# Kernel tuning notes

Hardware: AMD Instinct MI355X
Metric: run time of the kernel (lower is better)

## Reference

```python
import jax, jax.numpy as jnp
import numpy as np

# Mesh/packing dims: deltaV_packed.view(B, M, V, ndims) requires N = B*M*V
B, M, V = 2, 4, 40000
N = B * M * V            # 320_000 packed vertices
E = 960000               # ~3 edges per vertex (triangle mesh)
F_IN = 128               # n_input_features
LAT = 128                # latent_channels
NDIMS = 3
N_HIDDEN = 2             # n_f2f_hidden_layer


def graph_conv(x, edges, W0, b0, W1, b1):
    """pytorch3d-style GraphConv: w0(x) + sum_{j in N(i)} w1(x_j), undirected edges."""
    h0 = x @ W0 + b0                     # self term  [N, out]
    h1 = x @ W1 + b1                     # neighbor messages [N, out]
    src, dst = edges[:, 0], edges[:, 1]
    agg = jnp.zeros_like(h0).at[src].add(h1[dst]).at[dst].add(h1[src])
    return h0 + agg


def setup_inputs() -> dict:
    key = jax.random.key(0)
    ks = jax.random.split(key, 20)
    inp = {
        "features": jax.random.normal(ks[0], (N, F_IN), jnp.float32),
        "edges": jax.random.randint(ks[1], (E, 2), 0, N, dtype=jnp.int32),
    }
    # Layer dims: f2f first (F_IN->LAT), 2 hidden (LAT->LAT), f2v (LAT->NDIMS).
    dims = [(F_IN, LAT), (LAT, LAT), (LAT, LAT), (LAT, NDIMS)]
    for i, (din, dout) in enumerate(dims):
        kk = jax.random.split(ks[2 + i], 4)
        s = 1.0 / np.sqrt(din)
        inp[f"W0_{i}"] = jax.random.normal(kk[0], (din, dout), jnp.float32) * s
        inp[f"b0_{i}"] = jnp.zeros((dout,), jnp.float32)
        inp[f"W1_{i}"] = jax.random.normal(kk[1], (din, dout), jnp.float32) * s
        inp[f"b1_{i}"] = jnp.zeros((dout,), jnp.float32)
    return inp


def reference(features, edges,
              W0_0, b0_0, W1_0, b1_0,
              W0_1, b0_1, W1_1, b1_1,
              W0_2, b0_2, W1_2, b1_2,
              W0_3, b0_3, W1_3, b1_3):
    # Features2FeaturesResidual: first GC + 2 hidden GCs (ReLU each, norm='none'),
    # residual skip (identity since F_IN == LAT).
    h = jax.nn.relu(graph_conv(features, edges, W0_0, b0_0, W1_0, b1_0))
    h = jax.nn.relu(graph_conv(h, edges, W0_1, b0_1, W1_1, b1_1))
    h = jax.nn.relu(graph_conv(h, edges, W0_2, b0_2, W1_2, b1_2))
    h = h + features
    # f2v: GC(latent -> ndims), no activation
    deltaV = graph_conv(h, edges, W0_3, b0_3, W1_3, b1_3)
    return deltaV.reshape(B, M, V, NDIMS)
```

## Files before the change

kernel.cpp:

```cpp
#include <hip/hip_runtime.h>
#include <hip/hip_bf16.h>

#define NNODES 320000
#define NEDGES 960000

typedef __attribute__((ext_vector_type(8))) short short8;
typedef __attribute__((ext_vector_type(4))) float f32x4;

__device__ __forceinline__ float b2f(unsigned short u) {
    return __uint_as_float(((unsigned)u) << 16);
}
__device__ __forceinline__ unsigned short f2b(float f) {
    __hip_bfloat16 h = __float2bfloat16(f);
    union { __hip_bfloat16 h; unsigned short u; } cv;
    cv.h = h;
    return cv.u;
}


__global__ void k_zero(int* p, int n) {
    int i = blockIdx.x * blockDim.x + threadIdx.x;
    int s = gridDim.x * blockDim.x;
    for (; i < n; i += s) p[i] = 0;
}

__global__ void k_count(const int* __restrict__ edges, int* __restrict__ deg) {
    int i = blockIdx.x * blockDim.x + threadIdx.x;
    int s = gridDim.x * blockDim.x;
    for (; i < NEDGES; i += s) {
        int a = edges[2 * i], b = edges[2 * i + 1];
        atomicAdd(&deg[a], 1);
        atomicAdd(&deg[b], 1);
    }
}

#define SCAN_BLOCK 256
#define SCAN_ITEMS 8
#define SCAN_CHUNK 2048
#define SCAN_NB 157

__global__ void k_scan1(const int* __restrict__ deg, int* __restrict__ bsum) {
    __shared__ int sd[SCAN_BLOCK];
    int b = blockIdx.x, t = threadIdx.x;
    int base = b * SCAN_CHUNK + t * SCAN_ITEMS;
    int s = 0;
    for (int i = 0; i < SCAN_ITEMS; i++) {
        int g = base + i;
        if (g < NNODES) s += deg[g];
    }
    sd[t] = s;
    __syncthreads();
    for (int off = 128; off > 0; off >>= 1) {
        if (t < off) sd[t] += sd[t + off];
        __syncthreads();
    }
    if (t == 0) bsum[b] = sd[0];
}

__global__ void k_scan2(int* bsum, int* rowptr) {
    if (blockIdx.x == 0 && threadIdx.x == 0) {
        int run = 0;
        for (int b = 0; b < SCAN_NB; b++) {
            int v = bsum[b];
            bsum[b] = run;
            run += v;
        }
        rowptr[NNODES] = run;
    }
}

__global__ void k_scan3(int* __restrict__ deg_cursor, int* __restrict__ rowptr,
                        const int* __restrict__ bsum, float* __restrict__ degf) {
    __shared__ int sd[SCAN_BLOCK];
    int b = blockIdx.x, t = threadIdx.x;
    int base = b * SCAN_CHUNK + t * SCAN_ITEMS;
    int v[SCAN_ITEMS];
    int s = 0;
    for (int i = 0; i < SCAN_ITEMS; i++) {
        int g = base + i;
        v[i] = (g < NNODES) ? deg_cursor[g] : 0;
        s += v[i];
    }
    sd[t] = s;
    __syncthreads();
    for (int off = 1; off < SCAN_BLOCK; off <<= 1) {
        int x = (t >= off) ? sd[t - off] : 0;
        __syncthreads();
        sd[t] += x;
        __syncthreads();
    }
    int prefix = bsum[b] + (sd[t] - s);
    for (int i = 0; i < SCAN_ITEMS; i++) {
        int g = base + i;
        if (g < NNODES) {
            rowptr[g] = prefix;
            deg_cursor[g] = prefix;
            degf[g] = (float)v[i];
            prefix += v[i];
        }
    }
}

__global__ void k_fill(const int* __restrict__ edges, int* __restrict__ cursor,
                       int* __restrict__ adj) {
    int i = blockIdx.x * blockDim.x + threadIdx.x;
    int s = gridDim.x * blockDim.x;
    for (; i < NEDGES; i += s) {
        int a = edges[2 * i], b = edges[2 * i + 1];
        adj[atomicAdd(&cursor[a], 1)] = b;
        adj[atomicAdd(&cursor[b], 1)] = a;
    }
}


__global__ void k_cvt(const float* __restrict__ f, unsigned short* __restrict__ o,
                      long n4) {
    long i = (long)blockIdx.x * blockDim.x + threadIdx.x;
    long s = (long)gridDim.x * blockDim.x;
    for (; i < n4; i += s) {
        float4 v = *(const float4*)&f[i * 4];
        uint2 u;
        u.x = (unsigned)f2b(v.x) | ((unsigned)f2b(v.y) << 16);
        u.y = (unsigned)f2b(v.z) | ((unsigned)f2b(v.w) << 16);
        *(uint2*)&o[i * 4] = u;
    }
}

__global__ void k_cvtW(const float* __restrict__ W0, const float* __restrict__ W1,
                       unsigned short* __restrict__ Wt) {
    int idx = blockIdx.x * blockDim.x + threadIdx.x;
    if (idx >= 128 * 256) return;
    int c = idx >> 8, k = idx & 255;
    float v = (k < 128) ? W0[k * 128 + c] : W1[(k - 128) * 128 + c];
    Wt[idx] = f2b(v);
}


__global__ __launch_bounds__(256) void k_gather(
    const unsigned short* __restrict__ x, const int* __restrict__ rowptr,
    const int* __restrict__ adj, unsigned short* __restrict__ xsum) {
    int wid = (blockIdx.x * blockDim.x + threadIdx.x) >> 6;
    int lane = threadIdx.x & 63;
    int nw = (gridDim.x * blockDim.x) >> 6;
    for (int node = wid; node < NNODES; node += nw) {
        int s = rowptr[node], e = rowptr[node + 1];
        float a0 = 0.f, a1 = 0.f;
        for (int p = s; p < e; p += 8) {
            int cnt = e - p;
            if (cnt > 8) cnt = 8;
            int jv = (lane < cnt) ? adj[p + lane] : 0;
            unsigned vbuf[8];
#pragma unroll
            for (int q = 0; q < 8; ++q) {
                int j = __shfl(jv, q, 64);
                vbuf[q] = (q < cnt)
                              ? *(const unsigned*)&x[(size_t)j * 128 + lane * 2]
                              : 0u;
            }
#pragma unroll
            for (int q = 0; q < 8; ++q) {
                a0 += b2f(vbuf[q] & 0xffff);
                a1 += b2f(vbuf[q] >> 16);
            }
        }
        unsigned o = (unsigned)f2b(a0) | ((unsigned)f2b(a1) << 16);
        *(unsigned*)&xsum[(size_t)node * 128 + lane * 2] = o;
    }
}


#define XLD 136

template <int RES>
__global__ __launch_bounds__(256) void k_gemmF(
    const unsigned short* x, const unsigned short* __restrict__ xsum,
    const unsigned short* __restrict__ Wt, const float* __restrict__ b0,
    const float* __restrict__ b1, const float* __restrict__ degf,
    const unsigned short* __restrict__ feat, unsigned short* out) {
    __shared__ __align__(16) unsigned short Xs[64 * XLD];
    __shared__ __align__(16) unsigned short Ss[64 * XLD];

    int tid = threadIdx.x;
    int wave = tid >> 6, lane = tid & 63;
    int wm = wave >> 1, wn = wave & 1;
    int kg = (lane >> 4) << 3;
    int cl = lane & 15;

    short8 bF[8][4];
#pragma unroll
    for (int ks = 0; ks < 8; ++ks)
#pragma unroll
        for (int nf = 0; nf < 4; ++nf) {
            int c = wn * 64 + nf * 16 + cl;
            bF[ks][nf] = *(const short8*)&Wt[(size_t)c * 256 + ks * 32 + kg];
        }

    int rowBase = blockIdx.x * 64;
#pragma unroll
    for (int it = 0; it < 4; ++it) {
        int e = (it * 256 + tid) * 8;
        int r = e >> 7, k = e & 127;
        *(uint4*)&Xs[r * XLD + k] = *(const uint4*)&x[(size_t)(rowBase + r) * 128 + k];
        *(uint4*)&Ss[r * XLD + k] =
            *(const uint4*)&xsum[(size_t)(rowBase + r) * 128 + k];
    }
    __syncthreads();

    f32x4 acc[2][4];
#pragma unroll
    for (int i = 0; i < 2; i++)
#pragma unroll
        for (int j = 0; j < 4; j++) acc[i][j] = (f32x4){0.f, 0.f, 0.f, 0.f};

#pragma unroll
    for (int ks = 0; ks < 8; ++ks) {
        const unsigned short* src = (ks < 4) ? Xs : Ss;
        int kk = (ks & 3) * 32 + kg;
        short8 aF[2];
#pragma unroll
        for (int mf = 0; mf < 2; ++mf) {
            int r = wm * 32 + mf * 16 + cl;
            aF[mf] = *(const short8*)&src[r * XLD + kk];
        }
#pragma unroll
        for (int mf = 0; mf < 2; mf++)
#pragma unroll
            for (int nf = 0; nf < 4; nf++)
                acc[mf][nf] = __builtin_amdgcn_mfma_f32_16x16x32_bf16(
                    aF[mf], bF[ks][nf], acc[mf][nf], 0, 0, 0);
    }

#pragma unroll
    for (int nf = 0; nf < 4; nf++) {
        int c = wn * 64 + nf * 16 + cl;
        float bias0 = b0[c], bias1 = b1[c];
#pragma unroll
        for (int mf = 0; mf < 2; mf++) {
            int r0 = rowBase + wm * 32 + mf * 16 + ((lane >> 4) << 2);
            f32x4 d = acc[mf][nf];
#pragma unroll
            for (int q = 0; q < 4; q++) {
                int r = r0 + q;
                float v = d[q] + bias0 + degf[r] * bias1;
                v = fmaxf(v, 0.f);
                if (RES) v += b2f(feat[(size_t)r * 128 + c]);
                out[(size_t)r * 128 + c] = f2b(v);
            }
        }
    }
}


__global__ __launch_bounds__(256) void k_fin(
    const unsigned short* __restrict__ act, const unsigned short* __restrict__ hsum,
    const float* __restrict__ W0, const float* __restrict__ W1,
    const float* __restrict__ b0, const float* __restrict__ b1,
    const float* __restrict__ degf, float* __restrict__ out) {
    __shared__ __align__(16) unsigned short xa[64 * XLD];
    __shared__ __align__(16) unsigned short xs2[64 * XLD];
    __shared__ float Wf[768];
    __shared__ float ps[64][4][4];

    int tid = threadIdx.x;
    int nodeBase = blockIdx.x * 64;

    for (int idx = tid; idx < 384; idx += 256) {
        Wf[idx] = W0[idx];
        Wf[384 + idx] = W1[idx];
    }
#pragma unroll
    for (int it = 0; it < 4; ++it) {
        int e = (it * 256 + tid) * 8;
        int r = e >> 7, k = e & 127;
        *(uint4*)&xa[r * XLD + k] = *(const uint4*)&act[(size_t)(nodeBase + r) * 128 + k];
        *(uint4*)&xs2[r * XLD + k] =
            *(const uint4*)&hsum[(size_t)(nodeBase + r) * 128 + k];
    }
    __syncthreads();

    int n = tid >> 2, q = tid & 3;
    const unsigned short* src = (q < 2) ? xa : xs2;
    int kloc = (q & 1) * 64;
    float a0 = 0.f, a1 = 0.f, a2 = 0.f;
#pragma unroll
    for (int kk = 0; kk < 64; kk += 8) {
        uint4 v = *(const uint4*)&src[n * XLD + kloc + kk];
        unsigned vv[4] = {v.x, v.y, v.z, v.w};
#pragma unroll
        for (int t = 0; t < 4; t++) {
            int kgl = q * 64 + kk + 2 * t;
            float x0 = b2f(vv[t] & 0xffff), x1 = b2f(vv[t] >> 16);
            const float* w = &Wf[kgl * 3];
            a0 += x0 * w[0] + x1 * w[3];
            a1 += x0 * w[1] + x1 * w[4];
            a2 += x0 * w[2] + x1 * w[5];
        }
    }
    ps[n][q][0] = a0;
    ps[n][q][1] = a1;
    ps[n][q][2] = a2;
    __syncthreads();
    if (q == 0) {
        int node = nodeBase + n;
        float dg = degf[node];
#pragma unroll
        for (int c = 0; c < 3; c++) {
            float d = ps[n][0][c] + ps[n][1][c] + ps[n][2][c] + ps[n][3][c] +
                      b0[c] + dg * b1[c];
            out[(size_t)node * 3 + c] = d;
        }
    }
}


extern "C" void kernel_launch(void* const* d_in, const int* in_sizes, int n_in,
                              void* d_out, int out_size, void* d_ws, size_t ws_size,
                              hipStream_t stream) {
    const float* features = (const float*)d_in[0];
    const int* edges = (const int*)d_in[1];
    const float *W0[4], *B0[4], *W1[4], *B1[4];
    for (int i = 0; i < 4; i++) {
        W0[i] = (const float*)d_in[2 + 4 * i];
        B0[i] = (const float*)d_in[3 + 4 * i];
        W1[i] = (const float*)d_in[4 + 4 * i];
        B1[i] = (const float*)d_in[5 + 4 * i];
    }

    char* p = (char*)d_ws;
    auto alloc = [&](size_t bytes) {
        void* r = (void*)p;
        p += (bytes + 255) & ~(size_t)255;
        return r;
    };
    int* rowptr = (int*)alloc((NNODES + 1) * sizeof(int));
    int* cursor = (int*)alloc((NNODES + 1) * sizeof(int));
    float* degf = (float*)alloc(NNODES * sizeof(float));
    int* adj = (int*)alloc((size_t)2 * NEDGES * sizeof(int));
    int* bsum = (int*)alloc(1024);
    unsigned short* feat_bf = (unsigned short*)alloc((size_t)NNODES * 128 * 2);
    unsigned short* act = (unsigned short*)alloc((size_t)NNODES * 128 * 2);
    unsigned short* xsum = (unsigned short*)alloc((size_t)NNODES * 128 * 2);
    unsigned short* Wtb = (unsigned short*)alloc((size_t)3 * 128 * 256 * 2);

    k_zero<<<1024, 256, 0, stream>>>(cursor, NNODES + 1);
    k_count<<<2048, 256, 0, stream>>>(edges, cursor);
    k_scan1<<<SCAN_NB, SCAN_BLOCK, 0, stream>>>(cursor, bsum);
    k_scan2<<<1, 64, 0, stream>>>(bsum, rowptr);
    k_scan3<<<SCAN_NB, SCAN_BLOCK, 0, stream>>>(cursor, rowptr, bsum, degf);
    k_fill<<<2048, 256, 0, stream>>>(edges, cursor, adj);

    k_cvt<<<2048, 256, 0, stream>>>(features, feat_bf, (long)NNODES * 128 / 4);
    for (int l = 0; l < 3; l++)
        k_cvtW<<<128, 256, 0, stream>>>(W0[l], W1[l], Wtb + (size_t)l * 128 * 256);

    k_gather<<<8192, 256, 0, stream>>>(feat_bf, rowptr, adj, xsum);
    k_gemmF<0><<<NNODES / 64, 256, 0, stream>>>(feat_bf, xsum, Wtb, B0[0], B1[0],
                                                degf, nullptr, act);
    k_gather<<<8192, 256, 0, stream>>>(act, rowptr, adj, xsum);
    k_gemmF<0><<<NNODES / 64, 256, 0, stream>>>(act, xsum, Wtb + 128 * 256, B0[1],
                                                B1[1], degf, nullptr, act);
    k_gather<<<8192, 256, 0, stream>>>(act, rowptr, adj, xsum);
    k_gemmF<1><<<NNODES / 64, 256, 0, stream>>>(act, xsum, Wtb + 2 * 128 * 256,
                                                B0[2], B1[2], degf, feat_bf, act);
    k_gather<<<8192, 256, 0, stream>>>(act, rowptr, adj, xsum);
    k_fin<<<NNODES / 64, 256, 0, stream>>>(act, xsum, W0[3], W1[3], B0[3], B1[3],
                                           degf, (float*)d_out);
}
```

Before: 1.209 ms.

## Partition CSR build atomics, widen gather loads, use 8-wave GEMM blocks

The degree-count and fill kernels now split node ownership into 8 ranges, one per block group. Each block only performs atomics for endpoints in its range, which localizes contention and cache traffic, but every block now rereads all edges. The gather kernel has each lane load 16-byte rows for 2 neighbors in 4-neighbor groups, then combines the partial sums with xor shuffles. This replaces the old 4-byte-per-lane loads. The GEMM uses 512-thread blocks with 8 waves, each holding half the weight fragments, which reduces register use per wave so occupancy can rise.

New measurement: 1.153 ms. 4.6% less time.

```diff
diff --git a/kernel.cpp b/kernel.cpp
--- a/kernel.cpp
+++ b/kernel.cpp
@@ -3,6 +3,8 @@
 
 #define NNODES 320000
 #define NEDGES 960000
+#define NPART 8
+#define PARTSZ (NNODES / NPART)
 
 typedef __attribute__((ext_vector_type(8))) short short8;
 typedef __attribute__((ext_vector_type(4))) float f32x4;
@@ -25,12 +27,14 @@
 }
 
 __global__ void k_count(const int* __restrict__ edges, int* __restrict__ deg) {
-    int i = blockIdx.x * blockDim.x + threadIdx.x;
-    int s = gridDim.x * blockDim.x;
+    int r = blockIdx.x & (NPART - 1);
+    int lo = r * PARTSZ, hi = lo + PARTSZ;
+    int i = (blockIdx.x >> 3) * blockDim.x + threadIdx.x;
+    int s = (gridDim.x >> 3) * blockDim.x;
     for (; i < NEDGES; i += s) {
-        int a = edges[2 * i], b = edges[2 * i + 1];
-        atomicAdd(&deg[a], 1);
-        atomicAdd(&deg[b], 1);
+        int2 e = *(const int2*)&edges[2 * i];
+        if (e.x >= lo && e.x < hi) atomicAdd(&deg[e.x], 1);
+        if (e.y >= lo && e.y < hi) atomicAdd(&deg[e.y], 1);
     }
 }
 
@@ -103,12 +107,14 @@
 
 __global__ void k_fill(const int* __restrict__ edges, int* __restrict__ cursor,
                        int* __restrict__ adj) {
-    int i = blockIdx.x * blockDim.x + threadIdx.x;
-    int s = gridDim.x * blockDim.x;
+    int r = blockIdx.x & (NPART - 1);
+    int lo = r * PARTSZ, hi = lo + PARTSZ;
+    int i = (blockIdx.x >> 3) * blockDim.x + threadIdx.x;
+    int s = (gridDim.x >> 3) * blockDim.x;
     for (; i < NEDGES; i += s) {
-        int a = edges[2 * i], b = edges[2 * i + 1];
-        adj[atomicAdd(&cursor[a], 1)] = b;
-        adj[atomicAdd(&cursor[b], 1)] = a;
+        int2 e = *(const int2*)&edges[2 * i];
+        if (e.x >= lo && e.x < hi) adj[atomicAdd(&cursor[e.x], 1)] = e.y;
+        if (e.y >= lo && e.y < hi) adj[atomicAdd(&cursor[e.y], 1)] = e.x;
     }
 }
 
@@ -136,43 +142,59 @@
 }
 
 
+template <int L>
 __global__ __launch_bounds__(256) void k_gather(
     const unsigned short* __restrict__ x, const int* __restrict__ rowptr,
     const int* __restrict__ adj, unsigned short* __restrict__ xsum) {
     int wid = (blockIdx.x * blockDim.x + threadIdx.x) >> 6;
     int lane = threadIdx.x & 63;
     int nw = (gridDim.x * blockDim.x) >> 6;
+    int r = lane >> 4;
+    int cb = (lane & 15) * 8;
     for (int node = wid; node < NNODES; node += nw) {
         int s = rowptr[node], e = rowptr[node + 1];
-        float a0 = 0.f, a1 = 0.f;
+        float a[8];
+#pragma unroll
+        for (int q = 0; q < 8; q++) a[q] = 0.f;
         for (int p = s; p < e; p += 8) {
-            int cnt = e - p;
-            if (cnt > 8) cnt = 8;
-            int jv = (lane < cnt) ? adj[p + lane] : 0;
-            unsigned vbuf[8];
-#pragma unroll
-            for (int q = 0; q < 8; ++q) {
-                int j = __shfl(jv, q, 64);
-                vbuf[q] = (q < cnt)
-                              ? *(const unsigned*)&x[(size_t)j * 128 + lane * 2]
-                              : 0u;
+            int i0 = p + r, i1 = p + r + 4;
+            uint4 v0 = make_uint4(0, 0, 0, 0), v1 = make_uint4(0, 0, 0, 0);
+            if (i0 < e) {
+                int j = adj[i0];
+                v0 = *(const uint4*)&x[(size_t)j * 128 + cb];
             }
-#pragma unroll
-            for (int q = 0; q < 8; ++q) {
-                a0 += b2f(vbuf[q] & 0xffff);
-                a1 += b2f(vbuf[q] >> 16);
+            if (i1 < e) {
+                int j = adj[i1];
+                v1 = *(const uint4*)&x[(size_t)j * 128 + cb];
             }
-        }
-        unsigned o = (unsigned)f2b(a0) | ((unsigned)f2b(a1) << 16);
-        *(unsigned*)&xsum[(size_t)node * 128 + lane * 2] = o;
+            unsigned w0[4] = {v0.x, v0.y, v0.z, v0.w};
+            unsigned w1[4] = {v1.x, v1.y, v1.z, v1.w};
+#pragma unroll
+            for (int q = 0; q < 4; q++) {
+                a[2 * q] += b2f(w0[q] & 0xffff) + b2f(w1[q] & 0xffff);
+                a[2 * q + 1] += b2f(w0[q] >> 16) + b2f(w1[q] >> 16);
+            }
+        }
+#pragma unroll
+        for (int q = 0; q < 8; q++) a[q] += __shfl_xor(a[q], 16, 64);
+#pragma unroll
+        for (int q = 0; q < 8; q++) a[q] += __shfl_xor(a[q], 32, 64);
+        if (lane < 16) {
+            uint4 o;
+            o.x = (unsigned)f2b(a[0]) | ((unsigned)f2b(a[1]) << 16);
+            o.y = (unsigned)f2b(a[2]) | ((unsigned)f2b(a[3]) << 16);
+            o.z = (unsigned)f2b(a[4]) | ((unsigned)f2b(a[5]) << 16);
+            o.w = (unsigned)f2b(a[6]) | ((unsigned)f2b(a[7]) << 16);
+            *(uint4*)&xsum[(size_t)node * 128 + cb] = o;
+        }
     }
 }
 
 
 #define XLD 136
 
-template <int RES>
-__global__ __launch_bounds__(256) void k_gemmF(
+template <int RES, int L>
+__global__ __launch_bounds__(512, 4) void k_gemmF(
     const unsigned short* x, const unsigned short* __restrict__ xsum,
     const unsigned short* __restrict__ Wt, const float* __restrict__ b0,
     const float* __restrict__ b1, const float* __restrict__ degf,
@@ -182,23 +204,23 @@
 
     int tid = threadIdx.x;
     int wave = tid >> 6, lane = tid & 63;
-    int wm = wave >> 1, wn = wave & 1;
+    int wm = wave >> 2, wn = wave & 3;
     int kg = (lane >> 4) << 3;
     int cl = lane & 15;
 
-    short8 bF[8][4];
+    short8 bF[8][2];
 #pragma unroll
     for (int ks = 0; ks < 8; ++ks)
 #pragma unroll
-        for (int nf = 0; nf < 4; ++nf) {
-            int c = wn * 64 + nf * 16 + cl;
+        for (int nf = 0; nf < 2; ++nf) {
+            int c = wn * 32 + nf * 16 + cl;
             bF[ks][nf] = *(const short8*)&Wt[(size_t)c * 256 + ks * 32 + kg];
         }
 
     int rowBase = blockIdx.x * 64;
 #pragma unroll
-    for (int it = 0; it < 4; ++it) {
-        int e = (it * 256 + tid) * 8;
+    for (int it = 0; it < 2; ++it) {
+        int e = (it * 512 + tid) * 8;
         int r = e >> 7, k = e & 127;
         *(uint4*)&Xs[r * XLD + k] = *(const uint4*)&x[(size_t)(rowBase + r) * 128 + k];
         *(uint4*)&Ss[r * XLD + k] =
@@ -206,11 +228,11 @@
     }
     __syncthreads();
 
-    f32x4 acc[2][4];
+    f32x4 acc[2][2];
 #pragma unroll
     for (int i = 0; i < 2; i++)
 #pragma unroll
-        for (int j = 0; j < 4; j++) acc[i][j] = (f32x4){0.f, 0.f, 0.f, 0.f};
+        for (int j = 0; j < 2; j++) acc[i][j] = (f32x4){0.f, 0.f, 0.f, 0.f};
 
 #pragma unroll
     for (int ks = 0; ks < 8; ++ks) {
@@ -225,14 +247,14 @@
 #pragma unroll
         for (int mf = 0; mf < 2; mf++)
 #pragma unroll
-            for (int nf = 0; nf < 4; nf++)
+            for (int nf = 0; nf < 2; nf++)
                 acc[mf][nf] = __builtin_amdgcn_mfma_f32_16x16x32_bf16(
                     aF[mf], bF[ks][nf], acc[mf][nf], 0, 0, 0);
     }
 
 #pragma unroll
-    for (int nf = 0; nf < 4; nf++) {
-        int c = wn * 64 + nf * 16 + cl;
+    for (int nf = 0; nf < 2; nf++) {
+        int c = wn * 32 + nf * 16 + cl;
         float bias0 = b0[c], bias1 = b1[c];
 #pragma unroll
         for (int mf = 0; mf < 2; mf++) {
@@ -353,16 +375,16 @@
     for (int l = 0; l < 3; l++)
         k_cvtW<<<128, 256, 0, stream>>>(W0[l], W1[l], Wtb + (size_t)l * 128 * 256);
 
-    k_gather<<<8192, 256, 0, stream>>>(feat_bf, rowptr, adj, xsum);
-    k_gemmF<0><<<NNODES / 64, 256, 0, stream>>>(feat_bf, xsum, Wtb, B0[0], B1[0],
-                                                degf, nullptr, act);
-    k_gather<<<8192, 256, 0, stream>>>(act, rowptr, adj, xsum);
-    k_gemmF<0><<<NNODES / 64, 256, 0, stream>>>(act, xsum, Wtb + 128 * 256, B0[1],
-                                                B1[1], degf, nullptr, act);
-    k_gather<<<8192, 256, 0, stream>>>(act, rowptr, adj, xsum);
-    k_gemmF<1><<<NNODES / 64, 256, 0, stream>>>(act, xsum, Wtb + 2 * 128 * 256,
-                                                B0[2], B1[2], degf, feat_bf, act);
-    k_gather<<<8192, 256, 0, stream>>>(act, rowptr, adj, xsum);
+    k_gather<0><<<8192, 256, 0, stream>>>(feat_bf, rowptr, adj, xsum);
+    k_gemmF<0, 0><<<NNODES / 64, 512, 0, stream>>>(feat_bf, xsum, Wtb, B0[0], B1[0],
+                                                   degf, nullptr, act);
+    k_gather<1><<<8192, 256, 0, stream>>>(act, rowptr, adj, xsum);
+    k_gemmF<0, 1><<<NNODES / 64, 512, 0, stream>>>(act, xsum, Wtb + 128 * 256, B0[1],
+                                                   B1[1], degf, nullptr, act);
+    k_gather<2><<<8192, 256, 0, stream>>>(act, rowptr, adj, xsum);
+    k_gemmF<1, 2><<<NNODES / 64, 512, 0, stream>>>(act, xsum, Wtb + 2 * 128 * 256,
+                                                   B0[2], B1[2], degf, feat_bf, act);
+    k_gather<3><<<8192, 256, 0, stream>>>(act, rowptr, adj, xsum);
     k_fin<<<NNODES / 64, 256, 0, stream>>>(act, xsum, W0[3], W1[3], B0[3], B1[3],
                                            degf, (float*)d_out);
 }
```
